# Kernel tuning notes

Hardware: AMD Instinct MI355X
Metric: run time of the kernel (lower is better)

## Reference

```python
import jax, jax.numpy as jnp
import numpy as np

N_MEL = 80
N_CTX = 640  # n_text_channels + n_speaker_dim = 512 + 128
N_ATT = 128
TEMPERATURE = 1.0


def setup_inputs() -> dict:
    key = jax.random.key(0)
    ks = jax.random.split(key, 7)
    Tq, B, Tk = 512, 8, 256
    queries = jax.random.normal(ks[0], (Tq, B, N_MEL), dtype=jnp.float32)
    keys = jax.random.normal(ks[1], (Tk, B, N_CTX), dtype=jnp.float32)
    values = jax.random.normal(ks[2], (Tk, B, N_CTX), dtype=jnp.float32)
    # Linear weights (torch nn.Linear stores W as (out, in); y = x @ W.T)
    sq = 1.0 / np.sqrt(N_MEL)
    sk = 1.0 / np.sqrt(N_CTX)
    sv = 1.0 / np.sqrt(N_ATT)
    Wq = jax.random.normal(ks[3], (N_ATT, N_MEL), dtype=jnp.float32) * sq
    Wk = jax.random.normal(ks[4], (N_ATT, N_CTX), dtype=jnp.float32) * sk
    Wv = jax.random.normal(ks[5], (N_ATT, N_CTX), dtype=jnp.float32) * sk
    Wvec = jax.random.normal(ks[6], (N_ATT,), dtype=jnp.float32) * sv  # v: Linear(N_ATT, 1)
    return {"queries": queries, "keys": keys, "values": values,
            "Wq": Wq, "Wk": Wk, "Wv": Wv, "Wvec": Wvec}


def reference(queries, keys, values, Wq, Wk, Wv, Wvec):
    # Projections then time-major -> batch-major: (T,B,*) -> (B,T,C)
    q = jnp.einsum('tbi,ci->btc', queries, Wq)   # (B, Tq, C)
    k = jnp.einsum('tbi,ci->btc', keys, Wk)      # (B, Tk, C)
    v = jnp.einsum('tbi,ci->btc', values, Wv)    # (B, Tk, C)
    # Additive (Bahdanau) energies: broadcast add + tanh + v-dot reduce
    energy = jnp.tanh(q[:, :, None, :] + k[:, None, :, :])  # (B, Tq, Tk, C)
    attn = jnp.einsum('bqkc,c->bqk', energy, Wvec) / TEMPERATURE
    attn = jax.nn.softmax(attn, axis=2)          # softmax over Tk
    out = jnp.einsum('bqk,bkc->bqc', attn, v)    # (B, Tq, C)
    out = jnp.transpose(out, (0, 2, 1))          # (B, C, Tq)
    return (out, attn)
```

## Files before the change

### kernel.cpp

```cpp
#include <hip/hip_runtime.h>

#define TQ 512
#define TK 256
#define BB 8
#define CC 128

#define SCALE2L2E 2.8853900817779268f
#define L2E 1.4426950408889634f

__device__ __forceinline__ float fexp2(float x) { return __builtin_amdgcn_exp2f(x); }
__device__ __forceinline__ float frcp(float x)  { return __builtin_amdgcn_rcpf(x); }

typedef __fp16 h16x2 __attribute__((ext_vector_type(2)));
typedef __fp16 h16x4 __attribute__((ext_vector_type(4)));
typedef __fp16 h16x8 __attribute__((ext_vector_type(8)));
typedef _Float16 f16x8 __attribute__((ext_vector_type(8)));
typedef float f32x4 __attribute__((ext_vector_type(4)));

__device__ __forceinline__ f16x8 pack8(float4 lo, float4 hi) {
    h16x2 a0 = __builtin_amdgcn_cvt_pkrtz(lo.x, lo.y);
    h16x2 a1 = __builtin_amdgcn_cvt_pkrtz(lo.z, lo.w);
    h16x2 a2 = __builtin_amdgcn_cvt_pkrtz(hi.x, hi.y);
    h16x2 a3 = __builtin_amdgcn_cvt_pkrtz(hi.z, hi.w);
    h16x4 p0 = __builtin_shufflevector(a0, a1, 0, 1, 2, 3);
    h16x4 p1 = __builtin_shufflevector(a2, a3, 0, 1, 2, 3);
    h16x8 r = __builtin_shufflevector(p0, p1, 0, 1, 2, 3, 4, 5, 6, 7);
    return __builtin_bit_cast(f16x8, r);
}

__device__ __forceinline__ h16x4 pack4h(float4 v) {
    h16x2 lo = __builtin_amdgcn_cvt_pkrtz(v.x, v.y);
    h16x2 hi = __builtin_amdgcn_cvt_pkrtz(v.z, v.w);
    return __builtin_shufflevector(lo, hi, 0, 1, 2, 3);
}

#define CWK 10240
#define CWV 10240
#define CWQ 1536
#define CXQ 49152
#define CXK 163840
#define CXV 163840
#define CTOT (CWK + CWV + CWQ + CXQ + CXK + CXV)

__global__ __launch_bounds__(256) void convert_kernel(
    const float* __restrict__ Wk, const float* __restrict__ Wv,
    const float* __restrict__ Wq, const float* __restrict__ q_in,
    const float* __restrict__ k_in, const float* __restrict__ v_in,
    f16x8* __restrict__ Wk16s, f16x8* __restrict__ Wv16s,
    f16x8* __restrict__ Wq16s, f16x8* __restrict__ Xq16s,
    f16x8* __restrict__ Xk16s, f16x8* __restrict__ Xv16s)
{
    const int d = blockIdx.x * 256 + threadIdx.x;
    if (d >= CTOT) return;
    const f16x8 zero = {};

    const float* __restrict__ src;
    f16x8* __restrict__ dst;
    int dd, K;
    if (d < CWK)                         { dd = d; src = Wk; dst = Wk16s; K = 640; }
    else if (d < CWK + CWV)              { dd = d - CWK; src = Wv; dst = Wv16s; K = 640; }
    else if (d < CWK + CWV + CWQ)        { dd = d - CWK - CWV; src = Wq; dst = Wq16s; K = 80; }
    else if (d < CWK + CWV + CWQ + CXQ)  { dd = d - CWK - CWV - CWQ; src = q_in; dst = Xq16s; K = 80; }
    else if (d < CTOT - CXV)             { dd = d - CWK - CWV - CWQ - CXQ; src = k_in; dst = Xk16s; K = 640; }
    else                                 { dd = d - (CTOT - CXV); src = v_in; dst = Xv16s; K = 640; }

    const int nstep = (K == 640) ? 20 : 3;
    const int per = nstep * 64;
    const int tile = dd / per, rem = dd % per;
    const int s = rem >> 6, l = rem & 63;
    const int lr = l & 15, lk = l >> 4;
    const int r = tile * 16 + lr, k0 = s * 32 + lk * 8;
    if (K == 80 && k0 >= 80) { dst[dd] = zero; return; }
    float4 lo = *(const float4*)&src[(size_t)r * K + k0];
    float4 hi = *(const float4*)&src[(size_t)r * K + k0 + 4];
    dst[dd] = pack8(lo, hi);
}

__global__ __launch_bounds__(256) void proj_mfma(
    const _Float16* __restrict__ Wk16s, const _Float16* __restrict__ Wv16s,
    const _Float16* __restrict__ Wq16s, const _Float16* __restrict__ Xq16s,
    const _Float16* __restrict__ Xk16s, const _Float16* __restrict__ Xv16s,
    float* __restrict__ eqp, float* __restrict__ ekp, _Float16* __restrict__ v16s)
{
    const int tid = threadIdx.x;
    const int w = tid >> 6;
    const int l = tid & 63;
    const int lr = l & 15, lk = l >> 4;
    const int id = blockIdx.x;
    const int j = (id >> 1) * 4 + w;

    f32x4 acc0 = {0.f, 0.f, 0.f, 0.f};
    f32x4 acc1 = {0.f, 0.f, 0.f, 0.f};

    if ((id & 1) == 0) {
        const int tensor = j >> 9;
        const int jj = j & 511;
        const int rtile = jj >> 2;
        const int c0 = (jj & 3) * 32;
        const int r0 = rtile * 16;
        const _Float16* __restrict__ Xs = tensor ? Xv16s : Xk16s;
        const _Float16* __restrict__ Wt = tensor ? Wv16s : Wk16s;

        const _Float16* __restrict__ A0 = Xs + (size_t)rtile * 10240 + l * 8;
        const _Float16* __restrict__ B0 = Wt + (c0 >> 4) * 10240 + l * 8;
        const _Float16* __restrict__ B1 = B0 + 10240;

#pragma unroll
        for (int s = 0; s < 20; ++s) {
            f16x8 a = *(const f16x8*)(A0 + s * 512);
            f16x8 b0 = *(const f16x8*)(B0 + s * 512);
            f16x8 b1 = *(const f16x8*)(B1 + s * 512);
            acc0 = __builtin_amdgcn_mfma_f32_16x16x32_f16(a, b0, acc0, 0, 0, 0);
            acc1 = __builtin_amdgcn_mfma_f32_16x16x32_f16(a, b1, acc1, 0, 0, 0);
        }

        if (tensor == 0) {
#pragma unroll
            for (int jr = 0; jr < 4; ++jr) {
                int r = r0 + lk * 4 + jr;
                int t = r >> 3, bt = r & 7;
                ekp[((size_t)bt * CC + c0 + lr) * TK + t] = fexp2(SCALE2L2E * acc0[jr]);
                ekp[((size_t)bt * CC + c0 + 16 + lr) * TK + t] = fexp2(SCALE2L2E * acc1[jr]);
            }
        } else {
#pragma unroll
            for (int jr = 0; jr < 4; ++jr) {
                int r = r0 + lk * 4 + jr;
                int t = r >> 3, bt = r & 7;
                int base = bt * 32768 + (t >> 5) * 512 + ((t >> 3) & 3) * 128
                         + lr * 8 + (t & 7);
                v16s[base + (c0 >> 4) * 4096] = (_Float16)acc0[jr];
                v16s[base + ((c0 >> 4) + 1) * 4096] = (_Float16)acc1[jr];
            }
        }
    } else {
        const int rtile = j >> 2;
        const int c0 = (j & 3) * 32;

        const _Float16* __restrict__ A0 = Xq16s + (size_t)rtile * 1536 + l * 8;
        const _Float16* __restrict__ B0 = Wq16s + (c0 >> 4) * 1536 + l * 8;
        const _Float16* __restrict__ B1 = B0 + 1536;

#pragma unroll
        for (int s = 0; s < 3; ++s) {
            f16x8 a = *(const f16x8*)(A0 + s * 512);
            f16x8 bb0 = *(const f16x8*)(B0 + s * 512);
            f16x8 bb1 = *(const f16x8*)(B1 + s * 512);
            acc0 = __builtin_amdgcn_mfma_f32_16x16x32_f16(a, bb0, acc0, 0, 0, 0);
            acc1 = __builtin_amdgcn_mfma_f32_16x16x32_f16(a, bb1, acc1, 0, 0, 0);
        }

#pragma unroll
        for (int jr = 0; jr < 4; ++jr) {
            int r = rtile * 16 + lk * 4 + jr;
            int t = r >> 3, bt = r & 7;
            eqp[((size_t)bt * TQ + t) * CC + c0 + lr] = fexp2(SCALE2L2E * acc0[jr]);
            eqp[((size_t)bt * TQ + t) * CC + c0 + 16 + lr] = fexp2(SCALE2L2E * acc1[jr]);
        }
    }
}

__global__ __launch_bounds__(1024, 1) void attn_pv_kernel(
    const float* __restrict__ eqp, const float* __restrict__ ekp,
    const float* __restrict__ Wvec, const _Float16* __restrict__ v16s,
    float* __restrict__ attn_out, float* __restrict__ out)
{
    __shared__ float pa[4][64][52];
    __shared__ _Float16 pl[16][264];

    const int tid = threadIdx.x;
    const int lane = tid & 63;
    const int w = __builtin_amdgcn_readfirstlane(tid >> 6);
    const int g = w >> 2;
    const int qrt = w & 3;
    const int b = blockIdx.y;
    const int q0g = blockIdx.x * 16;
    const int q0 = q0g + g * 4;

    const float* __restrict__ qr0 = eqp + ((size_t)b * TQ + q0) * CC + qrt * 32;
    const float* __restrict__ qr1 = qr0 + CC;
    const float* __restrict__ qr2 = qr1 + CC;
    const float* __restrict__ qr3 = qr2 + CC;
    const float* __restrict__ kb = ekp + (size_t)b * CC * TK + (qrt * 32) * TK + lane * 4;
    const float* __restrict__ wvp = Wvec + qrt * 32;

    float sw = Wvec[lane] + Wvec[64 + lane];
#pragma unroll
    for (int m = 32; m >= 1; m >>= 1) sw += __shfl_xor(sw, m, 64);

    float a0[4] = {0.f, 0.f, 0.f, 0.f};
    float a1[4] = {0.f, 0.f, 0.f, 0.f};
    float a2[4] = {0.f, 0.f, 0.f, 0.f};
    float a3[4] = {0.f, 0.f, 0.f, 0.f};

    float4 k0 = *(const float4*)&kb[0 * TK];
    float4 k1 = *(const float4*)&kb[1 * TK];
    float4 k2 = *(const float4*)&kb[2 * TK];
    float4 k3 = *(const float4*)&kb[3 * TK];
    float4 wv = *(const float4*)&wvp[0];
    float4 qa = *(const float4*)&qr0[0];
    float4 qb = *(const float4*)&qr1[0];
    float4 qc = *(const float4*)&qr2[0];
    float4 qd = *(const float4*)&qr3[0];

    for (int c4 = 0; c4 < 32; c4 += 4) {
        float4 n0, n1, n2, n3, nwv, nqa, nqb, nqc, nqd;
        if (c4 + 4 < 32) {
            n0 = *(const float4*)&kb[(c4 + 4) * TK];
            n1 = *(const float4*)&kb[(c4 + 5) * TK];
            n2 = *(const float4*)&kb[(c4 + 6) * TK];
            n3 = *(const float4*)&kb[(c4 + 7) * TK];
            nwv = *(const float4*)&wvp[c4 + 4];
            nqa = *(const float4*)&qr0[c4 + 4];
            nqb = *(const float4*)&qr1[c4 + 4];
            nqc = *(const float4*)&qr2[c4 + 4];
            nqd = *(const float4*)&qr3[c4 + 4];
        }
#define CCOMP(KF, WW, EA, EB, EC, ED)                                   \
        a0[0] = fmaf(WW, frcp(fmaf(EA, KF.x, 1.f)), a0[0]);             \
        a0[1] = fmaf(WW, frcp(fmaf(EA, KF.y, 1.f)), a0[1]);             \
        a0[2] = fmaf(WW, frcp(fmaf(EA, KF.z, 1.f)), a0[2]);             \
        a0[3] = fmaf(WW, frcp(fmaf(EA, KF.w, 1.f)), a0[3]);             \
        a1[0] = fmaf(WW, frcp(fmaf(EB, KF.x, 1.f)), a1[0]);             \
        a1[1] = fmaf(WW, frcp(fmaf(EB, KF.y, 1.f)), a1[1]);             \
        a1[2] = fmaf(WW, frcp(fmaf(EB, KF.z, 1.f)), a1[2]);             \
        a1[3] = fmaf(WW, frcp(fmaf(EB, KF.w, 1.f)), a1[3]);             \
        a2[0] = fmaf(WW, frcp(fmaf(EC, KF.x, 1.f)), a2[0]);             \
        a2[1] = fmaf(WW, frcp(fmaf(EC, KF.y, 1.f)), a2[1]);             \
        a2[2] = fmaf(WW, frcp(fmaf(EC, KF.z, 1.f)), a2[2]);             \
        a2[3] = fmaf(WW, frcp(fmaf(EC, KF.w, 1.f)), a2[3]);             \
        a3[0] = fmaf(WW, frcp(fmaf(ED, KF.x, 1.f)), a3[0]);             \
        a3[1] = fmaf(WW, frcp(fmaf(ED, KF.y, 1.f)), a3[1]);             \
        a3[2] = fmaf(WW, frcp(fmaf(ED, KF.z, 1.f)), a3[2]);             \
        a3[3] = fmaf(WW, frcp(fmaf(ED, KF.w, 1.f)), a3[3]);
        CCOMP(k0, wv.x, qa.x, qb.x, qc.x, qd.x)
        CCOMP(k1, wv.y, qa.y, qb.y, qc.y, qd.y)
        CCOMP(k2, wv.z, qa.z, qb.z, qc.z, qd.z)
        CCOMP(k3, wv.w, qa.w, qb.w, qc.w, qd.w)
#undef CCOMP
        k0 = n0; k1 = n1; k2 = n2; k3 = n3;
        wv = nwv; qa = nqa; qb = nqb; qc = nqc; qd = nqd;
    }

    if (qrt != 0) {
        float* dstp = &pa[g][lane][(qrt - 1) * 16];
        *(float4*)(dstp + 0)  = make_float4(a0[0], a0[1], a0[2], a0[3]);
        *(float4*)(dstp + 4)  = make_float4(a1[0], a1[1], a1[2], a1[3]);
        *(float4*)(dstp + 8)  = make_float4(a2[0], a2[1], a2[2], a2[3]);
        *(float4*)(dstp + 12) = make_float4(a3[0], a3[1], a3[2], a3[3]);
    }
    __syncthreads();

    if (qrt == 0) {
#pragma unroll
        for (int p = 0; p < 3; ++p) {
            const float* srcp = &pa[g][lane][p * 16];
            float4 x0 = *(const float4*)(srcp + 0);
            float4 x1 = *(const float4*)(srcp + 4);
            float4 x2 = *(const float4*)(srcp + 8);
            float4 x3 = *(const float4*)(srcp + 12);
            a0[0] += x0.x; a0[1] += x0.y; a0[2] += x0.z; a0[3] += x0.w;
            a1[0] += x1.x; a1[1] += x1.y; a1[2] += x1.z; a1[3] += x1.w;
            a2[0] += x2.x; a2[1] += x2.y; a2[2] += x2.z; a2[3] += x2.w;
            a3[0] += x3.x; a3[1] += x3.y; a3[2] += x3.z; a3[3] += x3.w;
        }

        float sc0[4], sc1[4], sc2[4], sc3[4];
#pragma unroll
        for (int j = 0; j < 4; ++j) {
            sc0[j] = sw - 2.f * a0[j];
            sc1[j] = sw - 2.f * a1[j];
            sc2[j] = sw - 2.f * a2[j];
            sc3[j] = sw - 2.f * a3[j];
        }

        float m0 = fmaxf(fmaxf(sc0[0], sc0[1]), fmaxf(sc0[2], sc0[3]));
        float m1 = fmaxf(fmaxf(sc1[0], sc1[1]), fmaxf(sc1[2], sc1[3]));
        float m2 = fmaxf(fmaxf(sc2[0], sc2[1]), fmaxf(sc2[2], sc2[3]));
        float m3 = fmaxf(fmaxf(sc3[0], sc3[1]), fmaxf(sc3[2], sc3[3]));
#pragma unroll
        for (int m = 32; m >= 1; m >>= 1) {
            m0 = fmaxf(m0, __shfl_xor(m0, m, 64));
            m1 = fmaxf(m1, __shfl_xor(m1, m, 64));
            m2 = fmaxf(m2, __shfl_xor(m2, m, 64));
            m3 = fmaxf(m3, __shfl_xor(m3, m, 64));
        }
        float e0[4], e1[4], e2[4], e3[4];
        float s0 = 0.f, s1 = 0.f, s2 = 0.f, s3 = 0.f;
#pragma unroll
        for (int j = 0; j < 4; ++j) {
            e0[j] = fexp2((sc0[j] - m0) * L2E); s0 += e0[j];
            e1[j] = fexp2((sc1[j] - m1) * L2E); s1 += e1[j];
            e2[j] = fexp2((sc2[j] - m2) * L2E); s2 += e2[j];
            e3[j] = fexp2((sc3[j] - m3) * L2E); s3 += e3[j];
        }
#pragma unroll
        for (int m = 32; m >= 1; m >>= 1) {
            s0 += __shfl_xor(s0, m, 64);
            s1 += __shfl_xor(s1, m, 64);
            s2 += __shfl_xor(s2, m, 64);
            s3 += __shfl_xor(s3, m, 64);
        }
        const float r0 = frcp(s0), r1 = frcp(s1), r2 = frcp(s2), r3 = frcp(s3);

        const float4 p0 = make_float4(e0[0] * r0, e0[1] * r0, e0[2] * r0, e0[3] * r0);
        const float4 p1 = make_float4(e1[0] * r1, e1[1] * r1, e1[2] * r1, e1[3] * r1);
        const float4 p2 = make_float4(e2[0] * r2, e2[1] * r2, e2[2] * r2, e2[3] * r2);
        const float4 p3 = make_float4(e3[0] * r3, e3[1] * r3, e3[2] * r3, e3[3] * r3);

        float* __restrict__ po = attn_out + ((size_t)b * TQ + q0) * TK + lane * 4;
        *(float4*)(po + 0 * TK) = p0;
        *(float4*)(po + 1 * TK) = p1;
        *(float4*)(po + 2 * TK) = p2;
        *(float4*)(po + 3 * TK) = p3;

        *(h16x4*)&pl[g * 4 + 0][lane * 4] = pack4h(p0);
        *(h16x4*)&pl[g * 4 + 1][lane * 4] = pack4h(p1);
        *(h16x4*)&pl[g * 4 + 2][lane * 4] = pack4h(p2);
        *(h16x4*)&pl[g * 4 + 3][lane * 4] = pack4h(p3);
    }
    __syncthreads();

    if (w < 8) {
        const int lr = lane & 15, lk = lane >> 4;
        const _Float16* __restrict__ Vr = v16s + b * 32768 + w * 4096 + lane * 8;
        f32x4 acc = {0.f, 0.f, 0.f, 0.f};
#pragma unroll
        for (int s = 0; s < 8; ++s) {
            f16x8 a = *(const f16x8*)&pl[lr][s * 32 + lk * 8];
            f16x8 bv = *(const f16x8*)(Vr + s * 512);
            acc = __builtin_amdgcn_mfma_f32_16x16x32_f16(a, bv, acc, 0, 0, 0);
        }
        float4 o = make_float4(acc[0], acc[1], acc[2], acc[3]);
        *(float4*)&out[((size_t)b * CC + w * 16 + lr) * TQ + q0g + lk * 4] = o;
    }
}

extern "C" void kernel_launch(void* const* d_in, const int* in_sizes, int n_in,
                              void* d_out, int out_size, void* d_ws, size_t ws_size,
                              hipStream_t stream) {
    const float* queries = (const float*)d_in[0];
    const float* keys    = (const float*)d_in[1];
    const float* values  = (const float*)d_in[2];
    const float* Wq      = (const float*)d_in[3];
    const float* Wk      = (const float*)d_in[4];
    const float* Wv      = (const float*)d_in[5];
    const float* Wvec    = (const float*)d_in[6];

    float* out  = (float*)d_out;
    float* attn = out + BB * CC * TQ;

    float* ws = (float*)d_ws;
    float* eqp = ws;
    float* ekp = eqp + 4096 * CC;
    _Float16* v16s = (_Float16*)(ekp + 2048 * CC);
    _Float16* Wk16s = v16s + 8 * 32768;
    _Float16* Wv16s = Wk16s + 81920;
    _Float16* Wq16s = Wv16s + 81920;
    _Float16* Xq16s = Wq16s + 12288;
    _Float16* Xk16s = Xq16s + 393216;
    _Float16* Xv16s = Xk16s + 1310720;

    convert_kernel<<<dim3((CTOT + 255) / 256), 256, 0, stream>>>(
        Wk, Wv, Wq, queries, keys, values,
        (f16x8*)Wk16s, (f16x8*)Wv16s, (f16x8*)Wq16s,
        (f16x8*)Xq16s, (f16x8*)Xk16s, (f16x8*)Xv16s);
    proj_mfma<<<dim3(512), 256, 0, stream>>>(
        Wk16s, Wv16s, Wq16s, Xq16s, Xk16s, Xv16s, eqp, ekp, v16s);
    attn_pv_kernel<<<dim3(32, 8), 1024, 0, stream>>>(
        eqp, ekp, Wvec, v16s, attn, out);
}
```

Before: 41.47 us.

## Fuse key/value fp16 conversion into projection kernel via swizzled LDS staging

Stops pre-converting the large keys and values tensors to fp16 in the separate convert kernel. The projection kernel now loads the fp32 rows directly, converts them, and stages them in shared memory with an XOR-swizzled MFMA-friendly layout. This removes a full write and re-read of about 5 MB of fp16 intermediates and shrinks the convert launch. In exchange it adds an LDS staging phase, a block barrier, and shared-memory use per block.

```diff
diff --git a/kernel.cpp b/kernel.cpp
--- a/kernel.cpp
+++ b/kernel.cpp
@@ -38,20 +38,16 @@
 #define CWV 10240
 #define CWQ 1536
 #define CXQ 49152
-#define CXK 163840
-#define CXV 163840
-#define CTOT (CWK + CWV + CWQ + CXQ + CXK + CXV)
+#define CTOTA (CWK + CWV + CWQ + CXQ)
 
 __global__ __launch_bounds__(256) void convert_kernel(
     const float* __restrict__ Wk, const float* __restrict__ Wv,
     const float* __restrict__ Wq, const float* __restrict__ q_in,
-    const float* __restrict__ k_in, const float* __restrict__ v_in,
     f16x8* __restrict__ Wk16s, f16x8* __restrict__ Wv16s,
-    f16x8* __restrict__ Wq16s, f16x8* __restrict__ Xq16s,
-    f16x8* __restrict__ Xk16s, f16x8* __restrict__ Xv16s)
+    f16x8* __restrict__ Wq16s, f16x8* __restrict__ Xq16s)
 {
     const int d = blockIdx.x * 256 + threadIdx.x;
-    if (d >= CTOT) return;
+    if (d >= CTOTA) return;
     const f16x8 zero = {};
 
     const float* __restrict__ src;
@@ -60,9 +56,7 @@
     if (d < CWK)                         { dd = d; src = Wk; dst = Wk16s; K = 640; }
     else if (d < CWK + CWV)              { dd = d - CWK; src = Wv; dst = Wv16s; K = 640; }
     else if (d < CWK + CWV + CWQ)        { dd = d - CWK - CWV; src = Wq; dst = Wq16s; K = 80; }
-    else if (d < CWK + CWV + CWQ + CXQ)  { dd = d - CWK - CWV - CWQ; src = q_in; dst = Xq16s; K = 80; }
-    else if (d < CTOT - CXV)             { dd = d - CWK - CWV - CWQ - CXQ; src = k_in; dst = Xk16s; K = 640; }
-    else                                 { dd = d - (CTOT - CXV); src = v_in; dst = Xv16s; K = 640; }
+    else                                 { dd = d - CWK - CWV - CWQ; src = q_in; dst = Xq16s; K = 80; }
 
     const int nstep = (K == 640) ? 20 : 3;
     const int per = nstep * 64;
@@ -77,11 +71,13 @@
 }
 
 __global__ __launch_bounds__(256) void proj_mfma(
+    const float* __restrict__ k_in, const float* __restrict__ v_in,
     const _Float16* __restrict__ Wk16s, const _Float16* __restrict__ Wv16s,
     const _Float16* __restrict__ Wq16s, const _Float16* __restrict__ Xq16s,
-    const _Float16* __restrict__ Xk16s, const _Float16* __restrict__ Xv16s,
     float* __restrict__ eqp, float* __restrict__ ekp, _Float16* __restrict__ v16s)
 {
+    __shared__ _Float16 xs[20 * 520];
+
     const int tid = threadIdx.x;
     const int w = tid >> 6;
     const int l = tid & 63;
@@ -98,16 +94,29 @@
         const int rtile = jj >> 2;
         const int c0 = (jj & 3) * 32;
         const int r0 = rtile * 16;
-        const _Float16* __restrict__ Xs = tensor ? Xv16s : Xk16s;
+        const float* __restrict__ X = tensor ? v_in : k_in;
         const _Float16* __restrict__ Wt = tensor ? Wv16s : Wk16s;
 
-        const _Float16* __restrict__ A0 = Xs + (size_t)rtile * 10240 + l * 8;
+        for (int i = tid; i < 2560; i += 256) {
+            const int r = i / 160, kq = i % 160;
+            float4 v = *(const float4*)&X[(size_t)(r0 + r) * 640 + kq * 4];
+            const int k0 = kq * 4;
+            const int s = k0 >> 5;
+            const int lkw = (k0 >> 3) & 3;
+            const int jh = (k0 >> 2) & 1;
+            const int slot = (lkw * 16 + r) ^ lkw;
+            *(h16x4*)((char*)xs + s * 1040 + slot * 16 + jh * 8) = pack4h(v);
+        }
+        __syncthreads();
+
+        const int sigma = l ^ ((l >> 4) & 3);
+        const char* __restrict__ Abase = (const char*)xs + sigma * 16;
         const _Float16* __restrict__ B0 = Wt + (c0 >> 4) * 10240 + l * 8;
         const _Float16* __restrict__ B1 = B0 + 10240;
 
 #pragma unroll
         for (int s = 0; s < 20; ++s) {
-            f16x8 a = *(const f16x8*)(A0 + s * 512);
+            f16x8 a = *(const f16x8*)(Abase + s * 1040);
             f16x8 b0 = *(const f16x8*)(B0 + s * 512);
             f16x8 b1 = *(const f16x8*)(B1 + s * 512);
             acc0 = __builtin_amdgcn_mfma_f32_16x16x32_f16(a, b0, acc0, 0, 0, 0);
@@ -358,15 +367,12 @@
     _Float16* Wv16s = Wk16s + 81920;
     _Float16* Wq16s = Wv16s + 81920;
     _Float16* Xq16s = Wq16s + 12288;
-    _Float16* Xk16s = Xq16s + 393216;
-    _Float16* Xv16s = Xk16s + 1310720;
-
-    convert_kernel<<<dim3((CTOT + 255) / 256), 256, 0, stream>>>(
-        Wk, Wv, Wq, queries, keys, values,
-        (f16x8*)Wk16s, (f16x8*)Wv16s, (f16x8*)Wq16s,
-        (f16x8*)Xq16s, (f16x8*)Xk16s, (f16x8*)Xv16s);
+
+    convert_kernel<<<dim3(278), 256, 0, stream>>>(
+        Wk, Wv, Wq, queries,
+        (f16x8*)Wk16s, (f16x8*)Wv16s, (f16x8*)Wq16s, (f16x8*)Xq16s);
     proj_mfma<<<dim3(512), 256, 0, stream>>>(
-        Wk16s, Wv16s, Wq16s, Xq16s, Xk16s, Xv16s, eqp, ekp, v16s);
+        keys, values, Wk16s, Wv16s, Wq16s, Xq16s, eqp, ekp, v16s);
     attn_pv_kernel<<<dim3(32, 8), 1024, 0, stream>>>(
         eqp, ekp, Wvec, v16s, attn, out);
 }
```

Result: slower. 43.38 us (+4.6%).
